# Performance work log

Hardware: AMD Instinct MI355X
Metric: run time of the kernel (lower is better)

Reference implementation:

```python
import jax, jax.numpy as jnp
import numpy as np
import math

B, L, D, H = 2, 2048, 1024, 16
DK = D // H  # 64


def _lin(k, din, dout):
    kw, kb = jax.random.split(k)
    w = jax.random.normal(kw, (din, dout), dtype=jnp.float32) * 0.02
    b = jax.random.normal(kb, (dout,), dtype=jnp.float32) * 0.02
    return w, b


def setup_inputs() -> dict:
    key = jax.random.key(0)
    ks = jax.random.split(key, 12)
    wq, bq = _lin(ks[0], D, D)
    wk, bk = _lin(ks[1], D, D)
    wv, bv = _lin(ks[2], D, D)
    wo, bo = _lin(ks[3], D, D)
    whq, bhq = _lin(ks[4], DK, DK)
    whk, bhk = _lin(ks[5], DK, DK)
    whv, bhv = _lin(ks[6], DK, DK)
    who, bho = _lin(ks[7], DK, DK)
    return {
        "q_input": jax.random.normal(ks[8], (B, L, D), dtype=jnp.float32),
        "k_input": jax.random.normal(ks[9], (B, L, D), dtype=jnp.float32),
        "v_input": jax.random.normal(ks[10], (B, L, D), dtype=jnp.float32),
        "mask": jnp.ones((B, 1, L, L), dtype=jnp.int32),
        "wq": wq, "bq": bq, "wk": wk, "bk": bk, "wv": wv, "bv": bv,
        "wo": wo, "bo": bo,
        "whq": whq, "bhq": bhq, "whk": whk, "bhk": bhk,
        "whv": whv, "bhv": bhv, "who": who, "bho": bho,
    }


def reference(q_input, k_input, v_input, mask, wq, bq, wk, bk, wv, bv, wo, bo,
              whq, bhq, whk, bhk, whv, bhv, who, bho):
    scale = 1.0 / math.sqrt(DK)
    # Q/K/V projections -> [B, H, L, DK]
    Q = (q_input @ wq + bq).reshape(B, L, H, DK).transpose(0, 2, 1, 3)
    K = (k_input @ wk + bk).reshape(B, L, H, DK).transpose(0, 2, 1, 3)
    V = (v_input @ wv + bv).reshape(B, L, H, DK).transpose(0, 2, 1, 3)
    scores = jnp.einsum('bhqd,bhkd->bhqk', Q, K) * scale  # [B,H,L,L]
    neg = jnp.finfo(scores.dtype).min
    scores = jnp.where(mask == 0, neg, scores)
    probs = jax.nn.softmax(scores, axis=-1)  # dropout is identity in eval
    attn = jnp.einsum('bhqk,bhkd->bhqd', probs, V)
    heads = attn.transpose(0, 2, 1, 3)  # [B, L, H, DK]
    # Inter-head attention over the head dimension (size H) per position
    Qh = heads @ whq + bhq
    Kh = heads @ whk + bhk
    Vh = heads @ whv + bhv
    inter = jnp.einsum('blhd,blgd->blhg', Qh, Kh) * scale  # [B,L,H,H]
    iprobs = jax.nn.softmax(inter, axis=-1)
    mixed = jnp.einsum('blhg,blgd->blhd', iprobs, Vh)  # [B,L,H,DK]
    # note: inter_head_out is defined but unused in the original forward
    concat = mixed.reshape(B, L, D)
    return concat @ wo + bo
```

## Files before the change

### kernel.cpp

```cpp
#include <hip/hip_runtime.h>
#include <hip/hip_bf16.h>

typedef __bf16 bf16_t;
typedef __bf16 bf16x4 __attribute__((ext_vector_type(4)));
typedef __bf16 bf16x8 __attribute__((ext_vector_type(8)));
typedef float f32x4 __attribute__((ext_vector_type(4)));

typedef __attribute__((address_space(1))) unsigned char glob_u8;
typedef __attribute__((address_space(3))) unsigned char lds_u8;

__device__ __forceinline__ void load_lds16(const void* g, void* l) {
    __builtin_amdgcn_global_load_lds((glob_u8*)g, (lds_u8*)l, 16, 0, 0);
}

__global__ void prep1_kernel(const int* __restrict__ mask, int* __restrict__ flags,
                             const float* __restrict__ wq, const float* __restrict__ wk,
                             const float* __restrict__ wv, bf16_t* __restrict__ wqkvT)
{
    const int bid = blockIdx.x, t = threadIdx.x;
    if (bid < 2048) {
        int b = bid >> 10, qt = (bid >> 5) & 31, kt = bid & 31;
        int ok = 1;
#pragma unroll
        for (int i = 0; i < 16; i++) {
            int e = t + i * 256; int r = e >> 6, c = e & 63;
            ok &= (mask[((size_t)b * 2048 + qt * 64 + r) * 2048 + kt * 64 + c] != 0) ? 1 : 0;
        }
        ok = __syncthreads_and(ok);
        if (t == 0) flags[bid] = ok;
    } else {
        __shared__ bf16_t tile[64][65];
        int idx = bid - 2048;
        int z = idx >> 8, rem = idx & 255;
        const float* src = (z == 0) ? wq : (z == 1) ? wk : wv;
        bf16_t* dst = wqkvT + (size_t)z * 1048576;
        int rB = (rem >> 4) * 64, cB = (rem & 15) * 64;
#pragma unroll
        for (int i = 0; i < 16; i++) {
            int e = t + i * 256; int r = e >> 6, c = e & 63;
            tile[r][c] = (bf16_t)src[(size_t)(rB + r) * 1024 + cB + c];
        }
        __syncthreads();
#pragma unroll
        for (int i = 0; i < 16; i++) {
            int e = t + i * 256; int r = e >> 6, c = e & 63;
            dst[(size_t)(cB + r) * 1024 + rB + c] = tile[c][r];
        }
    }
}

__global__ void prep2_kernel(const float* __restrict__ wo, bf16_t* __restrict__ woT,
                             const float* __restrict__ s0, const float* __restrict__ s1,
                             const float* __restrict__ s2,
                             bf16_t* __restrict__ d0, bf16_t* __restrict__ d1, bf16_t* __restrict__ d2)
{
    const int bid = blockIdx.x, t = threadIdx.x;
    if (bid < 256) {
        __shared__ bf16_t tile[64][65];
        int rB = (bid >> 4) * 64, cB = (bid & 15) * 64;
#pragma unroll
        for (int i = 0; i < 16; i++) {
            int e = t + i * 256; int r = e >> 6, c = e & 63;
            tile[r][c] = (bf16_t)wo[(size_t)(rB + r) * 1024 + cB + c];
        }
        __syncthreads();
#pragma unroll
        for (int i = 0; i < 16; i++) {
            int e = t + i * 256; int r = e >> 6, c = e & 63;
            woT[(size_t)(cB + r) * 1024 + rB + c] = tile[c][r];
        }
    } else {
        int z = bid - 256;
        const float* src = (z == 0) ? s0 : (z == 1) ? s1 : s2;
        bf16_t* dst = (z == 0) ? d0 : (z == 1) ? d1 : d2;
#pragma unroll
        for (int i = 0; i < 16; i++) {
            int e = t + i * 256; int r = e >> 6, c = e & 63;
            dst[c * 64 + r] = (bf16_t)src[r * 64 + c];
        }
    }
}

#define GS 40

__global__ __launch_bounds__(256, 2) void gemm_qkv_kernel(
    const float* __restrict__ Aq, const float* __restrict__ Ak, const float* __restrict__ Av,
    const bf16_t* __restrict__ WT,
    const float* __restrict__ bq, const float* __restrict__ bk, const float* __restrict__ bv,
    bf16_t* __restrict__ outbase)
{
    __shared__ bf16_t As[128 * GS];
    __shared__ bf16_t Bs[128 * GS];
    const int z = blockIdx.z;
    const float* A    = (z == 0) ? Aq : (z == 1) ? Ak : Av;
    const bf16_t* Bt  = WT + (size_t)z * 1048576;
    const float* bia  = (z == 0) ? bq : (z == 1) ? bk : bv;
    bf16_t* out = outbase + (size_t)z * 4194304;

    const int t = threadIdx.x;
    const int w = t >> 6, lane = t & 63;
    const int lane15 = lane & 15, quad = lane >> 4;
    const int wr = w >> 1, wc = w & 1;
    const int rowBase = blockIdx.x * 128, colBase = blockIdx.y * 128;

    const int ar = t >> 1, ac = (t & 1) * 16;
    const int e0 = t * 8, e1 = (256 + t) * 8;
    const int r0 = e0 >> 5, c0 = e0 & 31;
    const int r1 = e1 >> 5, c1 = e1 & 31;

    f32x4 acc[4][4];
    f32x4 zf = {0.f, 0.f, 0.f, 0.f};
#pragma unroll
    for (int i = 0; i < 4; i++)
#pragma unroll
        for (int j = 0; j < 4; j++) acc[i][j] = zf;

    for (int k0 = 0; k0 < 1024; k0 += 32) {
        const float4* ap = (const float4*)(A + (size_t)(rowBase + ar) * 1024 + k0 + ac);
        float4 af4[4];
#pragma unroll
        for (int i = 0; i < 4; i++) af4[i] = ap[i];
        bf16x8 b0 = *(const bf16x8*)(Bt + (size_t)(colBase + r0) * 1024 + k0 + c0);
        bf16x8 b1 = *(const bf16x8*)(Bt + (size_t)(colBase + r1) * 1024 + k0 + c1);
        bf16x8 av0, av1;
#pragma unroll
        for (int i = 0; i < 4; i++) {
            bf16x8& dstv = (i < 2) ? av0 : av1;
            int base = (i & 1) * 4;
            dstv[base + 0] = (bf16_t)af4[i].x; dstv[base + 1] = (bf16_t)af4[i].y;
            dstv[base + 2] = (bf16_t)af4[i].z; dstv[base + 3] = (bf16_t)af4[i].w;
        }
        *(bf16x8*)(As + ar * GS + ac) = av0;
        *(bf16x8*)(As + ar * GS + ac + 8) = av1;
        *(bf16x8*)(Bs + r0 * GS + c0) = b0;
        *(bf16x8*)(Bs + r1 * GS + c1) = b1;
        __syncthreads();
        bf16x8 afr[4], bfr[4];
#pragma unroll
        for (int mi = 0; mi < 4; mi++)
            afr[mi] = *(const bf16x8*)(As + (wr * 64 + mi * 16 + lane15) * GS + quad * 8);
#pragma unroll
        for (int ni = 0; ni < 4; ni++)
            bfr[ni] = *(const bf16x8*)(Bs + (wc * 64 + ni * 16 + lane15) * GS + quad * 8);
#pragma unroll
        for (int mi = 0; mi < 4; mi++)
#pragma unroll
            for (int ni = 0; ni < 4; ni++)
                acc[mi][ni] = __builtin_amdgcn_mfma_f32_16x16x32_bf16(afr[mi], bfr[ni], acc[mi][ni], 0, 0, 0);
        __syncthreads();
    }

#pragma unroll
    for (int ni = 0; ni < 4; ni++) {
        int col = colBase + wc * 64 + ni * 16 + lane15;
        float bias = bia[col];
        int h = col >> 6, dk = col & 63;
#pragma unroll
        for (int mi = 0; mi < 4; mi++) {
#pragma unroll
            for (int r = 0; r < 4; r++) {
                int row = rowBase + wr * 64 + mi * 16 + quad * 4 + r;
                int b = row >> 11, l = row & 2047;
                float v = acc[mi][ni][r] + bias;
                size_t dst = (z < 2) ? ((((size_t)(b * 16 + h)) * 2048 + l) * 64 + dk)
                                     : ((((size_t)(b * 16 + h)) * 64 + dk) * 2048 + l);
                out[dst] = (bf16_t)v;
            }
        }
    }
}

__global__ __launch_bounds__(256, 2) void gemm_out_kernel(
    const bf16_t* __restrict__ A, const bf16_t* __restrict__ Bt,
    const float* __restrict__ bia, float* __restrict__ out)
{
    __shared__ bf16_t As[128 * 32];
    __shared__ bf16_t Bs[64 * 32];
    const int t = threadIdx.x;
    const int w = t >> 6, lane = t & 63;
    const int lane15 = lane & 15, quad = lane >> 4;
    const int wr = w >> 1, wc = w & 1;
    const int rowBase = blockIdx.x * 128, colBase = blockIdx.y * 64;

    const int brow = lane >> 2, bcol = (lane & 3) * 8;

    f32x4 acc[4][2];
    f32x4 zf = {0.f, 0.f, 0.f, 0.f};
#pragma unroll
    for (int i = 0; i < 4; i++)
#pragma unroll
        for (int j = 0; j < 2; j++) acc[i][j] = zf;

    for (int k0 = 0; k0 < 1024; k0 += 32) {
#pragma unroll
        for (int j = 0; j < 2; j++) {
            int chunk = w * 2 + j;
            load_lds16(A + (size_t)(rowBase + chunk * 16 + brow) * 1024 + k0 + bcol,
                       (char*)As + chunk * 1024);
        }
        {
            int chunk = w;
            load_lds16(Bt + (size_t)(colBase + chunk * 16 + brow) * 1024 + k0 + bcol,
                       (char*)Bs + chunk * 1024);
        }
        __syncthreads();
        bf16x8 afr[4], bfr[2];
#pragma unroll
        for (int mi = 0; mi < 4; mi++)
            afr[mi] = *(const bf16x8*)(As + (wr * 64 + mi * 16 + lane15) * 32 + quad * 8);
#pragma unroll
        for (int ni = 0; ni < 2; ni++)
            bfr[ni] = *(const bf16x8*)(Bs + (wc * 32 + ni * 16 + lane15) * 32 + quad * 8);
#pragma unroll
        for (int mi = 0; mi < 4; mi++)
#pragma unroll
            for (int ni = 0; ni < 2; ni++)
                acc[mi][ni] = __builtin_amdgcn_mfma_f32_16x16x32_bf16(afr[mi], bfr[ni], acc[mi][ni], 0, 0, 0);
        __syncthreads();
    }

#pragma unroll
    for (int ni = 0; ni < 2; ni++) {
        int col = colBase + wc * 32 + ni * 16 + lane15;
        float bias = bia[col];
#pragma unroll
        for (int mi = 0; mi < 4; mi++) {
#pragma unroll
            for (int r = 0; r < 4; r++) {
                int row = rowBase + wr * 64 + mi * 16 + quad * 4 + r;
                out[(size_t)row * 1024 + col] = acc[mi][ni][r] + bias;
            }
        }
    }
}

#define FS 72

__global__ __launch_bounds__(256, 2) void flash_kernel(
    const bf16_t* __restrict__ QKV, const int* __restrict__ mask,
    const int* __restrict__ flags, bf16_t* __restrict__ attnout)
{
    __shared__ bf16_t Ks[2][64 * FS];
    __shared__ bf16_t Vs[2][64 * FS];
    __shared__ bf16_t Ps[8 * 16 * FS];
    const int t = threadIdx.x, w = t >> 6, lane = t & 63;
    const int lane15 = lane & 15, quad = lane >> 4;
    const int qt = blockIdx.y, bh = blockIdx.x;
    const int b = bh >> 4, h = bh & 15;
    const bf16_t* Q  = QKV;
    const bf16_t* K  = QKV + 4194304;
    const bf16_t* Vt = QKV + 8388608;
    const int qrow0 = qt * 128 + w * 32;

    bf16x8 aq[2][2];
#pragma unroll
    for (int qf = 0; qf < 2; qf++) {
        const bf16_t* qb = Q + ((size_t)bh * 2048 + qrow0 + qf * 16 + lane15) * 64;
        aq[qf][0] = *(const bf16x8*)(qb + quad * 8);
        aq[qf][1] = *(const bf16x8*)(qb + 32 + quad * 8);
#pragma unroll
        for (int j = 0; j < 8; j++) {
            aq[qf][0][j] = (bf16_t)((float)aq[qf][0][j] * 0.125f);
            aq[qf][1][j] = (bf16_t)((float)aq[qf][1][j] * 0.125f);
        }
    }

    f32x4 zf = {0.f, 0.f, 0.f, 0.f};
    f32x4 o[2][4];
#pragma unroll
    for (int qf = 0; qf < 2; qf++)
#pragma unroll
        for (int df = 0; df < 4; df++) o[qf][df] = zf;
    f32x4 lsum[2] = {zf, zf};
    bf16_t* Pw0 = Ps + (w * 2 + 0) * 16 * FS;
    bf16_t* Pw1 = Ps + (w * 2 + 1) * 16 * FS;
    bf16x8 ones;
#pragma unroll
    for (int j = 0; j < 8; j++) ones[j] = (bf16_t)1.0f;

    const int e0 = t * 8, e1 = (256 + t) * 8;
    const int kr0 = e0 >> 6, kc0 = e0 & 63, kr1 = e1 >> 6, kc1 = e1 & 63;
    const int* flagrow = flags + (b * 32 + qt) * 32;
    const bf16_t* Kb  = K  + (size_t)bh * 131072;
    const bf16_t* Vtb = Vt + (size_t)bh * 131072;

    {
        bf16x8 k0v = *(const bf16x8*)(Kb  + (size_t)kr0 * 64 + kc0);
        bf16x8 k1v = *(const bf16x8*)(Kb  + (size_t)kr1 * 64 + kc1);
        bf16x8 v0v = *(const bf16x8*)(Vtb + (size_t)kr0 * 2048 + kc0);
        bf16x8 v1v = *(const bf16x8*)(Vtb + (size_t)kr1 * 2048 + kc1);
        *(bf16x8*)(Ks[0] + kr0 * FS + kc0) = k0v;
        *(bf16x8*)(Ks[0] + kr1 * FS + kc1) = k1v;
        *(bf16x8*)(Vs[0] + kr0 * FS + kc0) = v0v;
        *(bf16x8*)(Vs[0] + kr1 * FS + kc1) = v1v;
    }
    __syncthreads();

    for (int kt = 0; kt < 32; kt++) {
        const int cur = kt & 1, nxt = cur ^ 1;
        bf16x8 k0v, k1v, v0v, v1v;
        if (kt + 1 < 32) {
            int kn = (kt + 1) * 64;
            k0v = *(const bf16x8*)(Kb  + (size_t)(kn + kr0) * 64 + kc0);
            k1v = *(const bf16x8*)(Kb  + (size_t)(kn + kr1) * 64 + kc1);
            v0v = *(const bf16x8*)(Vtb + (size_t)kr0 * 2048 + kn + kc0);
            v1v = *(const bf16x8*)(Vtb + (size_t)kr1 * 2048 + kn + kc1);
        }

        f32x4 st[2][4];
#pragma unroll
        for (int kf = 0; kf < 4; kf++) {
            bf16x8 kb0 = *(const bf16x8*)(Ks[cur] + (kf * 16 + lane15) * FS + quad * 8);
            bf16x8 kb1 = *(const bf16x8*)(Ks[cur] + (kf * 16 + lane15) * FS + 32 + quad * 8);
#pragma unroll
            for (int qf = 0; qf < 2; qf++) {
                f32x4 a = zf;
                a = __builtin_amdgcn_mfma_f32_16x16x32_bf16(kb0, aq[qf][0], a, 0, 0, 0);
                a = __builtin_amdgcn_mfma_f32_16x16x32_bf16(kb1, aq[qf][1], a, 0, 0, 0);
                st[qf][kf] = a * 1.44269504f;
            }
        }
        if (kt + 1 < 32) {
            *(bf16x8*)(Ks[nxt] + kr0 * FS + kc0) = k0v;
            *(bf16x8*)(Ks[nxt] + kr1 * FS + kc1) = k1v;
            *(bf16x8*)(Vs[nxt] + kr0 * FS + kc0) = v0v;
            *(bf16x8*)(Vs[nxt] + kr1 * FS + kc1) = v1v;
        }
        if (!flagrow[kt]) {
#pragma unroll
            for (int qf = 0; qf < 2; qf++)
#pragma unroll
                for (int kf = 0; kf < 4; kf++)
#pragma unroll
                    for (int r = 0; r < 4; r++) {
                        int qrow = qrow0 + qf * 16 + lane15;
                        int kpos = kt * 64 + kf * 16 + quad * 4 + r;
                        if (mask[((size_t)b * 2048 + qrow) * 2048 + kpos] == 0)
                            st[qf][kf][r] = -1e30f;
                    }
        }
#pragma unroll
        for (int qf = 0; qf < 2; qf++) {
            bf16_t* Pq = qf ? Pw1 : Pw0;
#pragma unroll
            for (int kf = 0; kf < 4; kf++) {
                bf16x4 pv;
#pragma unroll
                for (int r = 0; r < 4; r++) pv[r] = (bf16_t)exp2f(st[qf][kf][r]);
                *(bf16x4*)(Pq + lane15 * FS + kf * 16 + quad * 4) = pv;
            }
        }
        bf16x8 pa[2][2];
        pa[0][0] = *(const bf16x8*)(Pw0 + lane15 * FS + quad * 8);
        pa[0][1] = *(const bf16x8*)(Pw0 + lane15 * FS + 32 + quad * 8);
        pa[1][0] = *(const bf16x8*)(Pw1 + lane15 * FS + quad * 8);
        pa[1][1] = *(const bf16x8*)(Pw1 + lane15 * FS + 32 + quad * 8);
#pragma unroll
        for (int qf = 0; qf < 2; qf++) {
            lsum[qf] = __builtin_amdgcn_mfma_f32_16x16x32_bf16(ones, pa[qf][0], lsum[qf], 0, 0, 0);
            lsum[qf] = __builtin_amdgcn_mfma_f32_16x16x32_bf16(ones, pa[qf][1], lsum[qf], 0, 0, 0);
        }
#pragma unroll
        for (int df = 0; df < 4; df++) {
            bf16x8 vb0 = *(const bf16x8*)(Vs[cur] + (df * 16 + lane15) * FS + quad * 8);
            bf16x8 vb1 = *(const bf16x8*)(Vs[cur] + (df * 16 + lane15) * FS + 32 + quad * 8);
#pragma unroll
            for (int qf = 0; qf < 2; qf++) {
                o[qf][df] = __builtin_amdgcn_mfma_f32_16x16x32_bf16(pa[qf][0], vb0, o[qf][df], 0, 0, 0);
                o[qf][df] = __builtin_amdgcn_mfma_f32_16x16x32_bf16(pa[qf][1], vb1, o[qf][df], 0, 0, 0);
            }
        }
        __syncthreads();
    }

#pragma unroll
    for (int qf = 0; qf < 2; qf++) {
        float lv = lsum[qf][0];
#pragma unroll
        for (int r = 0; r < 4; r++) {
            float inv = 1.0f / __shfl(lv, quad * 4 + r, 64);
            size_t row = (size_t)b * 2048 + qrow0 + qf * 16 + quad * 4 + r;
#pragma unroll
            for (int df = 0; df < 4; df++)
                attnout[(row * 16 + h) * 64 + df * 16 + lane15] = (bf16_t)(o[qf][df][r] * inv);
        }
    }
}

__global__ __launch_bounds__(256, 2) void interhead_kernel(
    const bf16_t* __restrict__ attn,
    const bf16_t* __restrict__ whqT, const float* __restrict__ bhq,
    const bf16_t* __restrict__ whkT, const float* __restrict__ bhk,
    const bf16_t* __restrict__ whvT, const float* __restrict__ bhv,
    bf16_t* __restrict__ concat)
{
    __shared__ bf16_t lds[4 * 4608];
    const int t = threadIdx.x, w = t >> 6, lane = t & 63;
    const int lane15 = lane & 15, quad = lane >> 4;
    bf16_t* Qh  = lds + w * 4608;
    bf16_t* Kh  = Qh + 1024;
    bf16_t* VhT = Kh + 1024;
    bf16_t* P16 = VhT + 2048;
    const int p = blockIdx.x * 4 + w;

    bf16x8 z8 = {(bf16_t)0.f, (bf16_t)0.f, (bf16_t)0.f, (bf16_t)0.f,
                 (bf16_t)0.f, (bf16_t)0.f, (bf16_t)0.f, (bf16_t)0.f};
    ((bf16x8*)P16)[lane] = z8;
#pragma unroll
    for (int i = 0; i < 4; i++) ((bf16x8*)VhT)[i * 64 + lane] = z8;

    const bf16_t* hb = attn + ((size_t)p * 16 + lane15) * 64;
    bf16x8 ha0 = *(const bf16x8*)(hb + quad * 8);
    bf16x8 ha1 = *(const bf16x8*)(hb + 32 + quad * 8);

    const bf16_t* Wt[3] = {whqT, whkT, whvT};
    const float*  Bb[3] = {bhq, bhk, bhv};
    f32x4 zf = {0.f, 0.f, 0.f, 0.f};
#pragma unroll
    for (int m3 = 0; m3 < 3; m3++) {
#pragma unroll
        for (int nf = 0; nf < 4; nf++) {
            f32x4 acc = zf;
            bf16x8 wb0 = *(const bf16x8*)(Wt[m3] + (nf * 16 + lane15) * 64 + quad * 8);
            bf16x8 wb1 = *(const bf16x8*)(Wt[m3] + (nf * 16 + lane15) * 64 + 32 + quad * 8);
            acc = __builtin_amdgcn_mfma_f32_16x16x32_bf16(ha0, wb0, acc, 0, 0, 0);
            acc = __builtin_amdgcn_mfma_f32_16x16x32_bf16(ha1, wb1, acc, 0, 0, 0);
            float bias = Bb[m3][nf * 16 + lane15];
#pragma unroll
            for (int r = 0; r < 4; r++) {
                float v = acc[r] + bias;
                if (m3 == 0) v *= 0.125f;
                if (m3 == 2) VhT[(nf * 16 + lane15) * 32 + quad * 4 + r] = (bf16_t)v;
                else if (m3 == 0) Qh[(quad * 4 + r) * 64 + nf * 16 + lane15] = (bf16_t)v;
                else Kh[(quad * 4 + r) * 64 + nf * 16 + lane15] = (bf16_t)v;
            }
        }
    }
    __syncthreads();

    bf16x8 qa0 = *(const bf16x8*)(Qh + lane15 * 64 + quad * 8);
    bf16x8 qa1 = *(const bf16x8*)(Qh + lane15 * 64 + 32 + quad * 8);
    bf16x8 kb0 = *(const bf16x8*)(Kh + lane15 * 64 + quad * 8);
    bf16x8 kb1 = *(const bf16x8*)(Kh + lane15 * 64 + 32 + quad * 8);
    f32x4 s = zf;
    s = __builtin_amdgcn_mfma_f32_16x16x32_bf16(qa0, kb0, s, 0, 0, 0);
    s = __builtin_amdgcn_mfma_f32_16x16x32_bf16(qa1, kb1, s, 0, 0, 0);
#pragma unroll
    for (int r = 0; r < 4; r++) {
        float v = s[r];
        float mx = v;
        mx = fmaxf(mx, __shfl_xor(mx, 1));
        mx = fmaxf(mx, __shfl_xor(mx, 2));
        mx = fmaxf(mx, __shfl_xor(mx, 4));
        mx = fmaxf(mx, __shfl_xor(mx, 8));
        float pv = __expf(v - mx);
        float sm = pv;
        sm += __shfl_xor(sm, 1);
        sm += __shfl_xor(sm, 2);
        sm += __shfl_xor(sm, 4);
        sm += __shfl_xor(sm, 8);
        P16[(quad * 4 + r) * 32 + lane15] = (bf16_t)(pv / sm);
    }
    __syncthreads();

    bf16x8 pa = *(const bf16x8*)(P16 + lane15 * 32 + quad * 8);
    bf16_t* outp = concat + (size_t)p * 1024;
#pragma unroll
    for (int df = 0; df < 4; df++) {
        bf16x8 vb = *(const bf16x8*)(VhT + (df * 16 + lane15) * 32 + quad * 8);
        f32x4 mix = zf;
        mix = __builtin_amdgcn_mfma_f32_16x16x32_bf16(pa, vb, mix, 0, 0, 0);
#pragma unroll
        for (int r = 0; r < 4; r++)
            outp[(quad * 4 + r) * 64 + df * 16 + lane15] = (bf16_t)mix[r];
    }
}

extern "C" void kernel_launch(void* const* d_in, const int* in_sizes, int n_in,
                              void* d_out, int out_size, void* d_ws, size_t ws_size,
                              hipStream_t stream)
{
    const float* q_in = (const float*)d_in[0];
    const float* k_in = (const float*)d_in[1];
    const float* v_in = (const float*)d_in[2];
    const int*   mask = (const int*)d_in[3];
    const float* wq = (const float*)d_in[4];
    const float* bq = (const float*)d_in[5];
    const float* wk = (const float*)d_in[6];
    const float* bk = (const float*)d_in[7];
    const float* wv = (const float*)d_in[8];
    const float* bv = (const float*)d_in[9];
    const float* wo = (const float*)d_in[10];
    const float* bo = (const float*)d_in[11];
    const float* whq = (const float*)d_in[12];
    const float* bhq = (const float*)d_in[13];
    const float* whk = (const float*)d_in[14];
    const float* bhk = (const float*)d_in[15];
    const float* whv = (const float*)d_in[16];
    const float* bhv = (const float*)d_in[17];
    float* out = (float*)d_out;

    char* ws = (char*)d_ws;
    bf16_t* qkvb  = (bf16_t*)ws;
    bf16_t* concat = qkvb;
    bf16_t* woT   = (bf16_t*)(ws + 8u * 1024 * 1024);
    bf16_t* whqT  = (bf16_t*)(ws + 10u * 1024 * 1024);
    bf16_t* whkT  = whqT + 4096;
    bf16_t* whvT  = whqT + 8192;
    bf16_t* attnb = (bf16_t*)d_out;
    bf16_t* wqkvT = (bf16_t*)((char*)d_out + 8u * 1024 * 1024);
    int*    flags = (int*)((char*)d_out + 14u * 1024 * 1024);

    prep1_kernel<<<2816, 256, 0, stream>>>(mask, flags, wq, wk, wv, wqkvT);
    gemm_qkv_kernel<<<dim3(32, 8, 3), 256, 0, stream>>>(q_in, k_in, v_in, wqkvT, bq, bk, bv, qkvb);
    flash_kernel<<<dim3(32, 16), 256, 0, stream>>>(qkvb, mask, flags, attnb);
    prep2_kernel<<<259, 256, 0, stream>>>(wo, woT, whq, whk, whv, whqT, whkT, whvT);
    interhead_kernel<<<1024, 256, 0, stream>>>(attnb, whqT, bhq, whkT, bhk, whvT, bhv, concat);
    gemm_out_kernel<<<dim3(32, 16), 256, 0, stream>>>(concat, woT, bo, out);
    (void)in_sizes; (void)n_in; (void)out_size; (void)ws_size;
}
```

Baseline: 307.9 us.

## Double-buffer QKV GEMM tiles via direct global-to-LDS loads with XOR swizzle

```diff
diff --git a/kernel.cpp b/kernel.cpp
--- a/kernel.cpp
+++ b/kernel.cpp
@@ -81,16 +81,14 @@
     }
 }
 
-#define GS 40
-
 __global__ __launch_bounds__(256, 2) void gemm_qkv_kernel(
     const float* __restrict__ Aq, const float* __restrict__ Ak, const float* __restrict__ Av,
     const bf16_t* __restrict__ WT,
     const float* __restrict__ bq, const float* __restrict__ bk, const float* __restrict__ bv,
     bf16_t* __restrict__ outbase)
 {
-    __shared__ bf16_t As[128 * GS];
-    __shared__ bf16_t Bs[128 * GS];
+    __shared__ float  Asf[2][128 * 32];
+    __shared__ bf16_t Bs[2][128 * 32];
     const int z = blockIdx.z;
     const float* A    = (z == 0) ? Aq : (z == 1) ? Ak : Av;
     const bf16_t* Bt  = WT + (size_t)z * 1048576;
@@ -103,10 +101,19 @@
     const int wr = w >> 1, wc = w & 1;
     const int rowBase = blockIdx.x * 128, colBase = blockIdx.y * 128;
 
-    const int ar = t >> 1, ac = (t & 1) * 16;
-    const int e0 = t * 8, e1 = (256 + t) * 8;
-    const int r0 = e0 >> 5, c0 = e0 & 31;
-    const int r1 = e1 >> 5, c1 = e1 & 31;
+    const int arow = lane >> 3;
+    const int achk = (lane & 7) ^ arow;
+    const int brow = lane >> 2;
+    const int bchk = (lane & 3) ^ ((brow >> 1) & 3);
+
+    const float*  aspA[4];
+#pragma unroll
+    for (int d = 0; d < 4; d++)
+        aspA[d] = A + (size_t)(rowBase + w * 32 + d * 8 + arow) * 1024 + achk * 4;
+    const bf16_t* aspB[2];
+#pragma unroll
+    for (int d = 0; d < 2; d++)
+        aspB[d] = Bt + (size_t)(colBase + w * 32 + d * 16 + brow) * 1024 + bchk * 8;
 
     f32x4 acc[4][4];
     f32x4 zf = {0.f, 0.f, 0.f, 0.f};
@@ -115,38 +122,55 @@
 #pragma unroll
         for (int j = 0; j < 4; j++) acc[i][j] = zf;
 
-    for (int k0 = 0; k0 < 1024; k0 += 32) {
-        const float4* ap = (const float4*)(A + (size_t)(rowBase + ar) * 1024 + k0 + ac);
-        float4 af4[4];
-#pragma unroll
-        for (int i = 0; i < 4; i++) af4[i] = ap[i];
-        bf16x8 b0 = *(const bf16x8*)(Bt + (size_t)(colBase + r0) * 1024 + k0 + c0);
-        bf16x8 b1 = *(const bf16x8*)(Bt + (size_t)(colBase + r1) * 1024 + k0 + c1);
-        bf16x8 av0, av1;
-#pragma unroll
-        for (int i = 0; i < 4; i++) {
-            bf16x8& dstv = (i < 2) ? av0 : av1;
-            int base = (i & 1) * 4;
-            dstv[base + 0] = (bf16_t)af4[i].x; dstv[base + 1] = (bf16_t)af4[i].y;
-            dstv[base + 2] = (bf16_t)af4[i].z; dstv[base + 3] = (bf16_t)af4[i].w;
-        }
-        *(bf16x8*)(As + ar * GS + ac) = av0;
-        *(bf16x8*)(As + ar * GS + ac + 8) = av1;
-        *(bf16x8*)(Bs + r0 * GS + c0) = b0;
-        *(bf16x8*)(Bs + r1 * GS + c1) = b1;
-        __syncthreads();
+    const int m7 = lane15 & 7;
+    const int m3b = (lane15 >> 1) & 3;
+
+#pragma unroll
+    for (int d = 0; d < 4; d++)
+        load_lds16(aspA[d], (char*)Asf[0] + (w * 32 + d * 8) * 128);
+#pragma unroll
+    for (int d = 0; d < 2; d++)
+        load_lds16(aspB[d], (char*)Bs[0] + (w * 32 + d * 16) * 64);
+    __syncthreads();
+
+    for (int kt = 0; kt < 32; kt++) {
+        const int cur = kt & 1, nxt = cur ^ 1;
+        if (kt < 31) {
+            const int k0 = (kt + 1) * 32;
+#pragma unroll
+            for (int d = 0; d < 4; d++)
+                load_lds16(aspA[d] + k0, (char*)Asf[nxt] + (w * 32 + d * 8) * 128);
+#pragma unroll
+            for (int d = 0; d < 2; d++)
+                load_lds16(aspB[d] + k0, (char*)Bs[nxt] + (w * 32 + d * 16) * 64);
+        }
+
         bf16x8 afr[4], bfr[4];
 #pragma unroll
-        for (int mi = 0; mi < 4; mi++)
-            afr[mi] = *(const bf16x8*)(As + (wr * 64 + mi * 16 + lane15) * GS + quad * 8);
-#pragma unroll
-        for (int ni = 0; ni < 4; ni++)
-            bfr[ni] = *(const bf16x8*)(Bs + (wc * 64 + ni * 16 + lane15) * GS + quad * 8);
+        for (int mi = 0; mi < 4; mi++) {
+            int row = wr * 64 + mi * 16 + lane15;
+            int p0 = (quad * 2) ^ m7, p1 = (quad * 2 + 1) ^ m7;
+            f32x4 u = *(const f32x4*)(Asf[cur] + row * 32 + p0 * 4);
+            f32x4 v = *(const f32x4*)(Asf[cur] + row * 32 + p1 * 4);
+            bf16x8 af;
+            af[0] = (bf16_t)u[0]; af[1] = (bf16_t)u[1];
+            af[2] = (bf16_t)u[2]; af[3] = (bf16_t)u[3];
+            af[4] = (bf16_t)v[0]; af[5] = (bf16_t)v[1];
+            af[6] = (bf16_t)v[2]; af[7] = (bf16_t)v[3];
+            afr[mi] = af;
+        }
+#pragma unroll
+        for (int ni = 0; ni < 4; ni++) {
+            int row = wc * 64 + ni * 16 + lane15;
+            int p = quad ^ m3b;
+            bfr[ni] = *(const bf16x8*)(Bs[cur] + row * 32 + p * 8);
+        }
 #pragma unroll
         for (int mi = 0; mi < 4; mi++)
 #pragma unroll
             for (int ni = 0; ni < 4; ni++)
                 acc[mi][ni] = __builtin_amdgcn_mfma_f32_16x16x32_bf16(afr[mi], bfr[ni], acc[mi][ni], 0, 0, 0);
+
         __syncthreads();
     }
 
```

Measured after the change: 318.5 us. 1.03x slower.
